# Kernel tuning notes

Hardware: AMD Instinct MI355X
Metric: run time of the kernel (lower is better)

The kernel has to match this reference:

```python
import jax, jax.numpy as jnp
import numpy as np

MAX_DUR = 8  # exclusive upper bound used when sampling durations


def setup_inputs() -> dict:
    key = jax.random.key(0)
    k1, k2 = jax.random.split(key)
    B, S, D = 16, 512, 384
    text_emb = jax.random.normal(k1, (B, S, D), dtype=jnp.float32)
    durations = jax.random.randint(k2, (B, S), 0, MAX_DUR, dtype=jnp.int32)
    return {"text_emb": text_emb, "durations": durations}


def reference(text_emb, durations):
    # text_emb: [B, S, D] float32; durations: [B, S] int32
    B, S, D = text_emb.shape
    max_len = S * MAX_DUR  # static padded length (jit-compatible stand-in for pad_sequence)
    # cumulative end offset of each token's expanded span: [B, S]
    cs = jnp.cumsum(durations, axis=1)
    t = jnp.arange(max_len, dtype=cs.dtype)  # output frame positions
    # for each output frame t, source token idx = first j with cs[j] > t
    idx = jax.vmap(lambda c: jnp.searchsorted(c, t, side="right"))(cs)  # [B, max_len]
    total = cs[:, -1:]                      # [B, 1] total expanded length per batch
    valid = t[None, :] < total              # [B, max_len] padding mask
    idx = jnp.clip(idx, 0, S - 1)
    # gather embeddings: [B, max_len, D]
    out = jnp.take_along_axis(text_emb, idx[:, :, None], axis=1)
    return jnp.where(valid[:, :, None], out, jnp.zeros((), dtype=text_emb.dtype))
```

## Files before the change

kernel.cpp:

```cpp
#include <hip/hip_runtime.h>


#define BB 16
#define SS 512
#define DD 384
#define D4 (DD / 4)
#define MAXLEN 4096
#define TILE_T 128
#define NT (MAXLEN / TILE_T)
#define NTHREADS 256

__global__ __launch_bounds__(NTHREADS)
void lr_fused_kernel(const float4* __restrict__ emb,
                     const int* __restrict__ dur,
                     float4* __restrict__ out) {
    __shared__ int cs[SS];
    __shared__ int idx_lds[TILE_T];

    const int blk  = blockIdx.x;
    const int b    = blk >> 5;
    const int tile = blk & (NT - 1);
    const int tid  = threadIdx.x;

    if (tid < 64) {
        const int* drow = dur + b * SS + tid * 8;
        int loc[8];
        int run = 0;
        #pragma unroll
        for (int j = 0; j < 8; ++j) { run += drow[j]; loc[j] = run; }
        int sc = run;
        #pragma unroll
        for (int off = 1; off < 64; off <<= 1) {
            int n = __shfl_up(sc, off, 64);
            if (tid >= off) sc += n;
        }
        const int base = sc - run;
        #pragma unroll
        for (int j = 0; j < 8; ++j) cs[tid * 8 + j] = base + loc[j];
    }
    __syncthreads();

    const int total = cs[SS - 1];
    const int t0 = tile * TILE_T;

    if (tid < TILE_T) {
        const int t = t0 + tid;
        int lo = 0, hi = SS;
        while (lo < hi) {
            int mid = (lo + hi) >> 1;
            if (cs[mid] <= t) lo = mid + 1; else hi = mid;
        }
        if (lo > SS - 1) lo = SS - 1;
        idx_lds[tid] = (t < total) ? lo : -1;
    }
    __syncthreads();

    const float4* embb = emb + b * SS * D4;
    float4* outb = out + (size_t)(b * MAXLEN + t0) * D4;
    const float4 z = make_float4(0.f, 0.f, 0.f, 0.f);
    #pragma unroll 4
    for (int j = tid; j < TILE_T * D4; j += NTHREADS) {
        const int tt  = j / D4;
        const int d4  = j - tt * D4;
        const int idx = idx_lds[tt];
        outb[j] = (idx >= 0) ? embb[idx * D4 + d4] : z;
    }
}

extern "C" void kernel_launch(void* const* d_in, const int* in_sizes, int n_in,
                              void* d_out, int out_size, void* d_ws, size_t ws_size,
                              hipStream_t stream) {
    const float* text_emb  = (const float*)d_in[0];
    const int*   durations = (const int*)d_in[1];
    float* out = (float*)d_out;

    lr_fused_kernel<<<BB * NT, NTHREADS, 0, stream>>>(
        (const float4*)text_emb, durations, (float4*)out);
}
```

Before: 135.9 us.

## Split into index-map prologue kernel and flat nontemporal gather kernel

Splits the fused kernel into two. A small prologue kernel computes the per-frame source index map once per batch and writes it to workspace. A flat one-element-per-thread gather kernel then reads that map and writes the output with nontemporal stores. This removes the redundant per-tile prefix sum and binary search and makes the write stream simpler. In exchange it adds a second launch, a serial prologue that runs on only 16 blocks, and a global round trip for the index map.

```diff
diff --git a/kernel.cpp b/kernel.cpp
--- a/kernel.cpp
+++ b/kernel.cpp
@@ -6,21 +6,14 @@
 #define DD 384
 #define D4 (DD / 4)
 #define MAXLEN 4096
-#define TILE_T 128
-#define NT (MAXLEN / TILE_T)
-#define NTHREADS 256
 
-__global__ __launch_bounds__(NTHREADS)
-void lr_fused_kernel(const float4* __restrict__ emb,
-                     const int* __restrict__ dur,
-                     float4* __restrict__ out) {
+typedef float f32x4 __attribute__((ext_vector_type(4)));
+
+__global__ __launch_bounds__(256)
+void lr_prologue_kernel(const int* __restrict__ dur, int* __restrict__ idxmap) {
     __shared__ int cs[SS];
-    __shared__ int idx_lds[TILE_T];
-
-    const int blk  = blockIdx.x;
-    const int b    = blk >> 5;
-    const int tile = blk & (NT - 1);
-    const int tid  = threadIdx.x;
+    const int b   = blockIdx.x;
+    const int tid = threadIdx.x;
 
     if (tid < 64) {
         const int* drow = dur + b * SS + tid * 8;
@@ -41,30 +34,31 @@
     __syncthreads();
 
     const int total = cs[SS - 1];
-    const int t0 = tile * TILE_T;
-
-    if (tid < TILE_T) {
-        const int t = t0 + tid;
+    int* omap = idxmap + b * MAXLEN;
+    for (int k = 0; k < MAXLEN / 256; ++k) {
+        const int t = k * 256 + tid;
         int lo = 0, hi = SS;
         while (lo < hi) {
             int mid = (lo + hi) >> 1;
             if (cs[mid] <= t) lo = mid + 1; else hi = mid;
         }
         if (lo > SS - 1) lo = SS - 1;
-        idx_lds[tid] = (t < total) ? lo : -1;
+        omap[t] = (t < total) ? lo : -1;
     }
-    __syncthreads();
+}
 
-    const float4* embb = emb + b * SS * D4;
-    float4* outb = out + (size_t)(b * MAXLEN + t0) * D4;
-    const float4 z = make_float4(0.f, 0.f, 0.f, 0.f);
-    #pragma unroll 4
-    for (int j = tid; j < TILE_T * D4; j += NTHREADS) {
-        const int tt  = j / D4;
-        const int d4  = j - tt * D4;
-        const int idx = idx_lds[tt];
-        outb[j] = (idx >= 0) ? embb[idx * D4 + d4] : z;
-    }
+__global__ __launch_bounds__(256)
+void lr_gather_kernel(const f32x4* __restrict__ emb,
+                      const int* __restrict__ idxmap,
+                      f32x4* __restrict__ out) {
+    const unsigned i = blockIdx.x * 256u + threadIdx.x;
+    const unsigned bt = i / D4;
+    const unsigned d4 = i - bt * D4;
+    const unsigned b  = bt >> 12;
+    const int idx = idxmap[bt];
+    f32x4 v = {0.f, 0.f, 0.f, 0.f};
+    if (idx >= 0) v = emb[(b * SS + (unsigned)idx) * D4 + d4];
+    __builtin_nontemporal_store(v, &out[i]);
 }
 
 extern "C" void kernel_launch(void* const* d_in, const int* in_sizes, int n_in,
@@ -74,6 +68,11 @@
     const int*   durations = (const int*)d_in[1];
     float* out = (float*)d_out;
 
-    lr_fused_kernel<<<BB * NT, NTHREADS, 0, stream>>>(
-        (const float4*)text_emb, durations, (float4*)out);
+    int* idxmap = (int*)d_ws;
+
+    lr_prologue_kernel<<<BB, 256, 0, stream>>>(durations, idxmap);
+
+    const int n4 = BB * MAXLEN * D4;
+    lr_gather_kernel<<<n4 / 256, 256, 0, stream>>>(
+        (const f32x4*)text_emb, idxmap, (f32x4*)out);
 }
```

New measurement: 137.3 us. About the same (+1.0%).
